# Kernel tuning notes

Measured on AMD Instinct MI355X. Metric: run time of the kernel, lower is better.

Reference implementation:

```python
import jax, jax.numpy as jnp
import numpy as np

N_NODES = 50000
N_EDGES = 800000
NFEAT, NHID, IN_HEAD, NCLASS, OUT_HEAD = 256, 16, 8, 47, 1
NEG_SLOPE = 0.2


def setup_inputs() -> dict:
    key = jax.random.key(0)
    ks = jax.random.split(key, 10)
    x = jax.random.normal(ks[0], (N_NODES, NFEAT), dtype=jnp.float32)
    edge_index = jax.random.randint(ks[1], (2, N_EDGES), 0, N_NODES, dtype=jnp.int64)
    W1 = jax.random.normal(ks[2], (NFEAT, IN_HEAD * NHID), dtype=jnp.float32) * 0.06
    a1_src = jax.random.normal(ks[3], (IN_HEAD, NHID), dtype=jnp.float32) * 0.25
    a1_dst = jax.random.normal(ks[4], (IN_HEAD, NHID), dtype=jnp.float32) * 0.25
    b1 = jax.random.normal(ks[5], (IN_HEAD * NHID,), dtype=jnp.float32) * 0.02
    W2 = jax.random.normal(ks[6], (IN_HEAD * NHID, NCLASS), dtype=jnp.float32) * 0.09
    a2_src = jax.random.normal(ks[7], (OUT_HEAD, NCLASS), dtype=jnp.float32) * 0.15
    a2_dst = jax.random.normal(ks[8], (OUT_HEAD, NCLASS), dtype=jnp.float32) * 0.15
    b2 = jax.random.normal(ks[9], (NCLASS,), dtype=jnp.float32) * 0.02
    return {"x": x, "edge_index": edge_index, "W1": W1, "a1_src": a1_src,
            "a1_dst": a1_dst, "b1": b1, "W2": W2, "a2_src": a2_src,
            "a2_dst": a2_dst, "b2": b2}


def _gat_layer(x, W, a_src, a_dst, b, src, dst, n_nodes, concat):
    # x: [N, F_in]; W: [F_in, H*C]; a_*: [H, C]
    H, C = a_src.shape
    h = (x @ W).reshape(n_nodes, H, C)                        # [N, H, C]
    # per-node partial attention logits, then gather per edge
    s_src = jnp.einsum('nhc,hc->nh', h, a_src)                # [N, H]
    s_dst = jnp.einsum('nhc,hc->nh', h, a_dst)                # [N, H]
    e = jax.nn.leaky_relu(s_src[src] + s_dst[dst], NEG_SLOPE) # [E, H]
    # segment softmax over destination node
    m = jax.ops.segment_max(e, dst, num_segments=n_nodes)     # [N, H]
    ex = jnp.exp(e - m[dst])
    denom = jax.ops.segment_sum(ex, dst, num_segments=n_nodes)
    alpha = ex / (denom[dst] + 1e-16)                         # [E, H]
    # weighted message aggregation (scatter-add)
    msg = alpha[:, :, None] * h[src]                          # [E, H, C]
    out = jax.ops.segment_sum(msg, dst, num_segments=n_nodes) # [N, H, C]
    out = out.reshape(n_nodes, H * C) if concat else out.mean(axis=1)
    return out + b


def reference(x, edge_index, W1, a1_src, a1_dst, b1, W2, a2_src, a2_dst, b2):
    n = x.shape[0]
    # PyG GATConv default: add self-loops
    loops = jnp.arange(n, dtype=edge_index.dtype)
    src = jnp.concatenate([edge_index[0], loops])
    dst = jnp.concatenate([edge_index[1], loops])
    # eval mode: dropout is identity
    h = _gat_layer(x, W1, a1_src, a1_dst, b1, src, dst, n, concat=True)
    h = jax.nn.elu(h)
    out = _gat_layer(h, W2, a2_src, a2_dst, b2, src, dst, n, concat=False)
    return jax.nn.log_softmax(out, axis=1)
```

## Files before the change

kernel.cpp:

```cpp
#include <hip/hip_runtime.h>
#include <hip/hip_fp16.h>

#define N_NODES 50000
#define N_EDGES 800000
#define E2 (N_EDGES + N_NODES)

#define BSHIFT 6
#define BMASK 63
#define NBUCK 782
#define EPB 4096
#define NBLKC 208

typedef _Float16 h8v __attribute__((ext_vector_type(8)));
typedef float f4v __attribute__((ext_vector_type(4)));


__global__ __launch_bounds__(256) void k_hist(const int* __restrict__ ei,
                                              int* __restrict__ gh) {
    __shared__ int h[NBUCK];
    int tid = threadIdx.x;
    for (int b = tid; b < NBUCK; b += 256) h[b] = 0;
    __syncthreads();
    int base = blockIdx.x * EPB;
    for (int i = tid; i < EPB; i += 256) {
        int e = base + i;
        if (e < E2) {
            int dst = (e < N_EDGES) ? ei[N_EDGES + e] : (e - N_EDGES);
            atomicAdd(&h[dst >> BSHIFT], 1);
        }
    }
    __syncthreads();
    for (int b = tid; b < NBUCK; b += 256) gh[blockIdx.x * NBUCK + b] = h[b];
}

__global__ __launch_bounds__(256) void k_colscan(int* __restrict__ gh,
                                                 int* __restrict__ tot) {
    int wave = threadIdx.x >> 6, lane = threadIdx.x & 63;
    int b = blockIdx.x * 4 + wave;
    if (b >= NBUCK) return;
    int carry = 0;
    for (int c = 0; c < NBLKC; c += 64) {
        int k = c + lane;
        int v = (k < NBLKC) ? gh[k * NBUCK + b] : 0;
        int x = v;
        #pragma unroll
        for (int o = 1; o < 64; o <<= 1) { int y = __shfl_up(x, o); if (lane >= o) x += y; }
        if (k < NBLKC) gh[k * NBUCK + b] = carry + x - v;
        carry += __shfl(x, 63);
    }
    if (lane == 0) tot[b] = carry;
}

__global__ __launch_bounds__(1024) void k_btot(const int* __restrict__ tot,
        int* __restrict__ boff, const float* __restrict__ W2, float* __restrict__ W2p) {
    int t = threadIdx.x;
    for (int i = t; i < 128 * 48; i += 1024) {
        int k = i / 48, c = i - k * 48;
        W2p[i] = (c < 47) ? W2[k * 47 + c] : 0.f;
    }
    int v = (t < NBUCK) ? tot[t] : 0;
    __shared__ int ws[16];
    int lane = t & 63, w = t >> 6;
    int x = v;
    #pragma unroll
    for (int o = 1; o < 64; o <<= 1) { int y = __shfl_up(x, o); if (lane >= o) x += y; }
    if (lane == 63) ws[w] = x;
    __syncthreads();
    if (t == 0) {
        #pragma unroll
        for (int j = 1; j < 16; ++j) ws[j] += ws[j - 1];
    }
    __syncthreads();
    int add = (w == 0) ? 0 : ws[w - 1];
    int excl = add + x - v;
    if (t < NBUCK) boff[t] = excl;
    if (t == NBUCK - 1) boff[NBUCK] = excl + v;
}

__global__ __launch_bounds__(256) void k_place(const int* __restrict__ ei,
        const int* __restrict__ gh, const int* __restrict__ boff,
        unsigned int* __restrict__ brec) {
    __shared__ int sbase[NBUCK];
    __shared__ int cnt[NBUCK];
    int tid = threadIdx.x;
    for (int b = tid; b < NBUCK; b += 256) {
        sbase[b] = boff[b] + gh[blockIdx.x * NBUCK + b];
        cnt[b] = 0;
    }
    __syncthreads();
    int base = blockIdx.x * EPB;
    for (int i = tid; i < EPB; i += 256) {
        int e = base + i;
        if (e < E2) {
            int src, dst;
            if (e < N_EDGES) { src = ei[e]; dst = ei[N_EDGES + e]; }
            else             { src = dst = e - N_EDGES; }
            int b = dst >> BSHIFT;
            int r = atomicAdd(&cnt[b], 1);
            brec[sbase[b] + r] = ((unsigned int)(dst & BMASK) << 16) | (unsigned int)src;
        }
    }
}

__global__ __launch_bounds__(256) void k_finalize(const unsigned int* __restrict__ brec,
        const int* __restrict__ boff, unsigned short* __restrict__ csr_src,
        int* __restrict__ offs) {
    int B = blockIdx.x;
    int tid = threadIdx.x;
    int base = boff[B];
    int total = boff[B + 1] - base;
    __shared__ int hist[64], cur[64];
    __shared__ unsigned short stage[2048];
    if (tid < 64) hist[tid] = 0;
    __syncthreads();
    const unsigned int* bp = brec + base;
    for (int i = tid; i < total; i += 256) atomicAdd(&hist[bp[i] >> 16], 1);
    __syncthreads();
    if (tid < 64) {
        int v = hist[tid];
        int x = v;
        #pragma unroll
        for (int o = 1; o < 64; o <<= 1) { int y = __shfl_up(x, o); if (tid >= o) x += y; }
        int excl = x - v;
        cur[tid] = excl;
        int n = B * 64 + tid;
        if (n < N_NODES) offs[n] = base + excl;
    }
    if (B == NBUCK - 1 && tid == 0) offs[N_NODES] = boff[NBUCK];
    __syncthreads();
    if (total <= 2048) {
        for (int i = tid; i < total; i += 256) {
            unsigned int r = bp[i];
            int p = atomicAdd(&cur[r >> 16], 1);
            stage[p] = (unsigned short)(r & 0xFFFFu);
        }
        __syncthreads();
        for (int i = tid; i < total; i += 256) csr_src[base + i] = stage[i];
    } else {
        for (int i = tid; i < total; i += 256) {
            unsigned int r = bp[i];
            int p = atomicAdd(&cur[r >> 16], 1);
            csr_src[base + p] = (unsigned short)(r & 0xFFFFu);
        }
    }
}


__global__ void k_prepw1(const float* __restrict__ W1, _Float16* __restrict__ W1T) {
    int i = blockIdx.x * 256 + threadIdx.x;
    if (i >= 128 * 256) return;
    int c = i >> 8, k = i & 255;
    W1T[i] = (_Float16)W1[k * 128 + c];
}


__global__ __launch_bounds__(128) void k_gemm1(const float* __restrict__ x,
        const _Float16* __restrict__ W1T, _Float16* __restrict__ h1h) {
    int lane = threadIdx.x & 63;
    int wv = threadIdx.x >> 6;
    int rowbase = blockIdx.x * 64 + wv * 32;
    int r0 = lane & 15;
    int kg = lane >> 4;
    f4v acc[2][8];
    #pragma unroll
    for (int i = 0; i < 2; ++i)
        #pragma unroll
        for (int j = 0; j < 8; ++j) acc[i][j] = (f4v)0.f;

    #pragma unroll 1
    for (int kt = 0; kt < 256; kt += 32) {
        h8v a[2];
        #pragma unroll
        for (int rf = 0; rf < 2; ++rf) {
            int row = rowbase + rf * 16 + r0;
            if (row >= N_NODES) row = N_NODES - 1;
            const float* ap = x + (size_t)row * 256 + kt + kg * 8;
            float4 lo = *(const float4*)ap;
            float4 hi = *(const float4*)(ap + 4);
            h8v t;
            t[0] = (_Float16)lo.x; t[1] = (_Float16)lo.y;
            t[2] = (_Float16)lo.z; t[3] = (_Float16)lo.w;
            t[4] = (_Float16)hi.x; t[5] = (_Float16)hi.y;
            t[6] = (_Float16)hi.z; t[7] = (_Float16)hi.w;
            a[rf] = t;
        }
        #pragma unroll
        for (int cf = 0; cf < 8; ++cf) {
            h8v b = *(const h8v*)(W1T + (size_t)(cf * 16 + r0) * 256 + kt + kg * 8);
            acc[0][cf] = __builtin_amdgcn_mfma_f32_16x16x32_f16(a[0], b, acc[0][cf], 0, 0, 0);
            acc[1][cf] = __builtin_amdgcn_mfma_f32_16x16x32_f16(a[1], b, acc[1][cf], 0, 0, 0);
        }
    }
    #pragma unroll
    for (int rf = 0; rf < 2; ++rf) {
        #pragma unroll
        for (int r = 0; r < 4; ++r) {
            int row = rowbase + rf * 16 + kg * 4 + r;
            if (row < N_NODES) {
                _Float16* orow = h1h + (size_t)row * 128 + r0;
                #pragma unroll
                for (int cf = 0; cf < 8; ++cf)
                    orow[cf * 16] = (_Float16)acc[rf][cf][r];
            }
        }
    }
}


__global__ void k_logits1(const __half* __restrict__ h1h,
                          const float* __restrict__ a1s, const float* __restrict__ a1d,
                          float* __restrict__ s1s, float* __restrict__ s1d) {
    int idx = blockIdx.x * blockDim.x + threadIdx.x;
    if (idx >= N_NODES * 8) return;
    int n = idx >> 3, h = idx & 7;
    const __half2* hp2 = (const __half2*)(h1h + (size_t)n * 128 + h * 16);
    float ss = 0.f, sd = 0.f;
    #pragma unroll
    for (int c2 = 0; c2 < 8; ++c2) {
        float2 v = __half22float2(hp2[c2]);
        ss += v.x * a1s[h * 16 + 2 * c2] + v.y * a1s[h * 16 + 2 * c2 + 1];
        sd += v.x * a1d[h * 16 + 2 * c2] + v.y * a1d[h * 16 + 2 * c2 + 1];
    }
    s1s[idx] = ss;
    s1d[idx] = sd;
}


__global__ __launch_bounds__(256) void k_agg1(const __half* __restrict__ h1h,
        const float* __restrict__ s1s, const float* __restrict__ s1d,
        const int* __restrict__ offs, const unsigned short* __restrict__ csr_src,
        const float* __restrict__ b1, float* __restrict__ h2o) {
    int wave = threadIdx.x >> 6;
    int lane = threadIdx.x & 63;
    int n = blockIdx.x * 4 + wave;
    int beg = offs[n];
    int deg = offs[n + 1] - beg;

    int h = lane & 7;
    int slot = lane >> 3;
    int hd = lane >> 3;
    float sdh = s1d[n * 8 + h];

    float dsum = 0.f;
    float accx = 0.f, accy = 0.f;
    for (int chunk = 0; chunk < deg; chunk += 8) {
        int i = chunk + slot;
        int esrc = csr_src[beg + ((i < deg) ? i : (deg - 1))];
        float aN = 0.f;
        if (i < deg) {
            float e = s1s[esrc * 8 + h] + sdh;
            e = (e > 0.f) ? e : 0.2f * e;
            aN = __expf(e);
            dsum += aN;
        }
        int   srcs[8];
        float as[8];
        #pragma unroll
        for (int s = 0; s < 8; ++s) {
            srcs[s] = __shfl(esrc, s * 8);
            as[s]   = __shfl(aN, s * 8 + hd);
        }
        __half2 v[8];
        #pragma unroll
        for (int s = 0; s < 8; ++s)
            v[s] = *(const __half2*)(h1h + (size_t)srcs[s] * 128 + 2 * lane);
        #pragma unroll
        for (int s = 0; s < 8; ++s) {
            float2 vf = __half22float2(v[s]);
            accx += as[s] * vf.x;
            accy += as[s] * vf.y;
        }
    }
    dsum += __shfl_xor(dsum, 8);
    dsum += __shfl_xor(dsum, 16);
    dsum += __shfl_xor(dsum, 32);
    float rd = 1.f / __shfl(dsum, hd);

    float v0 = accx * rd + b1[2 * lane];
    v0 = (v0 > 0.f) ? v0 : (__expf(v0) - 1.f);
    float v1 = accy * rd + b1[2 * lane + 1];
    v1 = (v1 > 0.f) ? v1 : (__expf(v1) - 1.f);
    *(float2*)(h2o + (size_t)n * 128 + 2 * lane) = make_float2(v0, v1);
}


__global__ __launch_bounds__(256) void k_gemm2(const float* __restrict__ h2,
        const float* __restrict__ W2p,
        const float* __restrict__ a2s, const float* __restrict__ a2d,
        __half* __restrict__ g2h, float* __restrict__ s2s, float* __restrict__ s2d) {
    int n = blockIdx.x * 256 + threadIdx.x;
    bool valid = (n < N_NODES);
    int nn = valid ? n : (N_NODES - 1);
    const float* hrow = h2 + (size_t)nn * 128;
    float4 acc[12];
    #pragma unroll
    for (int j = 0; j < 12; ++j) acc[j] = make_float4(0.f, 0.f, 0.f, 0.f);
    #pragma unroll 1
    for (int k = 0; k < 128; k += 4) {
        float4 hv = *(const float4*)(hrow + k);
        float hk[4] = {hv.x, hv.y, hv.z, hv.w};
        #pragma unroll
        for (int kk = 0; kk < 4; ++kk) {
            const float* wrow = W2p + (size_t)(k + kk) * 48;
            #pragma unroll
            for (int j = 0; j < 12; ++j) {
                float4 wv = *(const float4*)(wrow + j * 4);
                acc[j].x += hk[kk] * wv.x;
                acc[j].y += hk[kk] * wv.y;
                acc[j].z += hk[kk] * wv.z;
                acc[j].w += hk[kk] * wv.w;
            }
        }
    }
    float vs = 0.f, vd = 0.f;
    #pragma unroll
    for (int j = 0; j < 12; ++j) {
        int c = j * 4;
        vs += acc[j].x * a2s[c + 0]; vd += acc[j].x * a2d[c + 0];
        vs += acc[j].y * a2s[c + 1]; vd += acc[j].y * a2d[c + 1];
        vs += acc[j].z * a2s[c + 2]; vd += acc[j].z * a2d[c + 2];
        if (j < 11) { vs += acc[j].w * a2s[c + 3]; vd += acc[j].w * a2d[c + 3]; }
    }
    if (valid) {
        __half2* orow = (__half2*)(g2h + (size_t)n * 48);
        #pragma unroll
        for (int j = 0; j < 12; ++j) {
            orow[j * 2 + 0] = __floats2half2_rn(acc[j].x, acc[j].y);
            orow[j * 2 + 1] = __floats2half2_rn(acc[j].z, acc[j].w);
        }
        s2s[n] = vs;
        s2d[n] = vd;
    }
}


__global__ __launch_bounds__(256) void k_agg2(const __half* __restrict__ g2h,
        const float* __restrict__ s2s, const float* __restrict__ s2d,
        const int* __restrict__ offs, const unsigned short* __restrict__ csr_src,
        const float* __restrict__ b2, float* __restrict__ outp) {
    int wave = threadIdx.x >> 6, lane = threadIdx.x & 63;
    int n = blockIdx.x * 4 + wave;
    int beg = offs[n];
    int deg = offs[n + 1] - beg;
    float sdn = s2d[n];
    int c = (lane < 47) ? lane : 47;

    float dsum = 0.f;
    float acc = 0.f;
    for (int chunk = 0; chunk < deg; chunk += 64) {
        int i = chunk + lane;
        int esrc = csr_src[beg + ((i < deg) ? i : (deg - 1))];
        float aN = 0.f;
        if (i < deg) {
            float e = s2s[esrc] + sdn;
            e = (e > 0.f) ? e : 0.2f * e;
            aN = __expf(e);
            dsum += aN;
        }
        int lim = deg - chunk; if (lim > 64) lim = 64;
        for (int g = 0; g < lim; g += 8) {
            int   srcs[8];
            float as[8];
            #pragma unroll
            for (int s = 0; s < 8; ++s) {
                srcs[s] = __shfl(esrc, g + s);
                as[s]   = __shfl(aN, g + s);
            }
            __half v[8];
            #pragma unroll
            for (int s = 0; s < 8; ++s) v[s] = g2h[(size_t)srcs[s] * 48 + c];
            #pragma unroll
            for (int s = 0; s < 8; ++s) acc += as[s] * __half2float(v[s]);
        }
    }
    #pragma unroll
    for (int o = 32; o; o >>= 1) dsum += __shfl_xor(dsum, o);
    acc *= 1.f / dsum;

    float l = (lane < 47) ? acc + b2[lane] : -1e30f;
    float rm = l;
    #pragma unroll
    for (int o = 32; o; o >>= 1) rm = fmaxf(rm, __shfl_xor(rm, o));
    float p = (lane < 47) ? __expf(l - rm) : 0.f;
    float ps = p;
    #pragma unroll
    for (int o = 32; o; o >>= 1) ps += __shfl_xor(ps, o);
    float lse = rm + __logf(ps);
    if (lane < 47) outp[(size_t)n * 47 + lane] = l - lse;
}


extern "C" void kernel_launch(void* const* d_in, const int* in_sizes, int n_in,
                              void* d_out, int out_size, void* d_ws, size_t ws_size,
                              hipStream_t stream) {
    const float* x   = (const float*)d_in[0];
    const int*   ei  = (const int*)d_in[1];
    const float* W1  = (const float*)d_in[2];
    const float* a1s = (const float*)d_in[3];
    const float* a1d = (const float*)d_in[4];
    const float* b1  = (const float*)d_in[5];
    const float* W2  = (const float*)d_in[6];
    const float* a2s = (const float*)d_in[7];
    const float* a2d = (const float*)d_in[8];
    const float* b2  = (const float*)d_in[9];
    float* outp = (float*)d_out;

    char* ws = (char*)d_ws;
    size_t off = 0;
    auto alloc = [&](size_t bytes) -> void* {
        void* p = ws + off;
        off += (bytes + 255) & ~(size_t)255;
        return p;
    };
    int* gh      = (int*)alloc((size_t)NBLKC * NBUCK * 4);
    int* tot     = (int*)alloc((size_t)NBUCK * 4);
    int* boff    = (int*)alloc((size_t)(NBUCK + 1) * 4);
    unsigned int* brec = (unsigned int*)alloc((size_t)E2 * 4);
    unsigned short* csr_src = (unsigned short*)alloc((size_t)E2 * 2);
    int* offs    = (int*)alloc((size_t)(N_NODES + 1) * 4);
    __half* h1h  = (__half*)alloc((size_t)N_NODES * 128 * 2);
    float* s1s   = (float*)alloc((size_t)N_NODES * 8 * 4);
    float* s1d   = (float*)alloc((size_t)N_NODES * 8 * 4);
    float* h2    = (float*)alloc((size_t)N_NODES * 128 * 4);
    __half* g2h  = (__half*)alloc((size_t)N_NODES * 48 * 2);
    float* s2s   = (float*)alloc((size_t)N_NODES * 4);
    float* s2d   = (float*)alloc((size_t)N_NODES * 4);
    float* W2p   = (float*)alloc((size_t)128 * 48 * 4);
    _Float16* W1T = (_Float16*)alloc((size_t)128 * 256 * 2);

    (void)in_sizes; (void)n_in; (void)out_size; (void)ws_size;

    k_prepw1<<<128, 256, 0, stream>>>(W1, W1T);
    k_hist<<<NBLKC, 256, 0, stream>>>(ei, gh);
    k_colscan<<<(NBUCK + 3) / 4, 256, 0, stream>>>(gh, tot);
    k_btot<<<1, 1024, 0, stream>>>(tot, boff, W2, W2p);
    k_place<<<NBLKC, 256, 0, stream>>>(ei, gh, boff, brec);
    k_finalize<<<NBUCK, 256, 0, stream>>>(brec, boff, csr_src, offs);

    k_gemm1<<<(N_NODES + 63) / 64, 128, 0, stream>>>(x, W1T, (_Float16*)h1h);
    k_logits1<<<(N_NODES * 8 + 255) / 256, 256, 0, stream>>>(h1h, a1s, a1d, s1s, s1d);
    k_agg1<<<N_NODES / 4, 256, 0, stream>>>(h1h, s1s, s1d, offs, csr_src, b1, h2);

    k_gemm2<<<(N_NODES + 255) / 256, 256, 0, stream>>>(h2, W2p, a2s, a2d, g2h, s2s, s2d);
    k_agg2<<<N_NODES / 4, 256, 0, stream>>>(g2h, s2s, s2d, offs, csr_src, b2, outp);
}
```

Measured before the change: 181.5 us.

## Split layer-1 aggregation per head, store fp16 head-major h2, fuse W1 prep

The layer-1 aggregation now launches one wave per (node, head): lanes gather 16 channels across four edge groups at once, and the partial sums are reduced with shuffles. The layer-1 output is stored as fp16 in a head-major layout, and gemm2 is changed to read that layout. W1 transpose prep moves into an extra block of the histogram kernel, which removes one launch. This raises parallelism for low-degree nodes and halves h2 traffic. In exchange, the edge list and logits are re-read once per head, the h1h gathers become 32-byte scattered reads, and h2 loses some precision.

```diff
diff --git a/kernel.cpp b/kernel.cpp
--- a/kernel.cpp
+++ b/kernel.cpp
@@ -16,7 +16,14 @@
 
 
 __global__ __launch_bounds__(256) void k_hist(const int* __restrict__ ei,
-                                              int* __restrict__ gh) {
+        int* __restrict__ gh, const float* __restrict__ W1, _Float16* __restrict__ W1T) {
+    if (blockIdx.x == NBLKC) {
+        for (int i = threadIdx.x; i < 128 * 256; i += 256) {
+            int c = i >> 8, k = i & 255;
+            W1T[i] = (_Float16)W1[k * 128 + c];
+        }
+        return;
+    }
     __shared__ int h[NBUCK];
     int tid = threadIdx.x;
     for (int b = tid; b < NBUCK; b += 256) h[b] = 0;
@@ -143,14 +150,6 @@
             csr_src[base + p] = (unsigned short)(r & 0xFFFFu);
         }
     }
-}
-
-
-__global__ void k_prepw1(const float* __restrict__ W1, _Float16* __restrict__ W1T) {
-    int i = blockIdx.x * 256 + threadIdx.x;
-    if (i >= 128 * 256) return;
-    int c = i >> 8, k = i & 255;
-    W1T[i] = (_Float16)W1[k * 128 + c];
 }
 
 
@@ -229,86 +228,81 @@
 __global__ __launch_bounds__(256) void k_agg1(const __half* __restrict__ h1h,
         const float* __restrict__ s1s, const float* __restrict__ s1d,
         const int* __restrict__ offs, const unsigned short* __restrict__ csr_src,
-        const float* __restrict__ b1, float* __restrict__ h2o) {
+        const float* __restrict__ b1, __half* __restrict__ h2s) {
     int wave = threadIdx.x >> 6;
     int lane = threadIdx.x & 63;
-    int n = blockIdx.x * 4 + wave;
+    int s = blockIdx.x & 7;
+    int n = (blockIdx.x >> 3) * 4 + wave;
     int beg = offs[n];
     int deg = offs[n + 1] - beg;
-
-    int h = lane & 7;
-    int slot = lane >> 3;
-    int hd = lane >> 3;
-    float sdh = s1d[n * 8 + h];
+    int c = lane & 15;
+    int grp = lane >> 4;
+    float sdh = s1d[n * 8 + s];
 
     float dsum = 0.f;
-    float accx = 0.f, accy = 0.f;
-    for (int chunk = 0; chunk < deg; chunk += 8) {
-        int i = chunk + slot;
+    float acc = 0.f;
+    for (int chunk = 0; chunk < deg; chunk += 64) {
+        int i = chunk + lane;
         int esrc = csr_src[beg + ((i < deg) ? i : (deg - 1))];
         float aN = 0.f;
         if (i < deg) {
-            float e = s1s[esrc * 8 + h] + sdh;
+            float e = s1s[esrc * 8 + s] + sdh;
             e = (e > 0.f) ? e : 0.2f * e;
             aN = __expf(e);
             dsum += aN;
         }
-        int   srcs[8];
-        float as[8];
-        #pragma unroll
-        for (int s = 0; s < 8; ++s) {
-            srcs[s] = __shfl(esrc, s * 8);
-            as[s]   = __shfl(aN, s * 8 + hd);
-        }
-        __half2 v[8];
-        #pragma unroll
-        for (int s = 0; s < 8; ++s)
-            v[s] = *(const __half2*)(h1h + (size_t)srcs[s] * 128 + 2 * lane);
-        #pragma unroll
-        for (int s = 0; s < 8; ++s) {
-            float2 vf = __half22float2(v[s]);
-            accx += as[s] * vf.x;
-            accy += as[s] * vf.y;
-        }
-    }
-    dsum += __shfl_xor(dsum, 8);
-    dsum += __shfl_xor(dsum, 16);
-    dsum += __shfl_xor(dsum, 32);
-    float rd = 1.f / __shfl(dsum, hd);
-
-    float v0 = accx * rd + b1[2 * lane];
-    v0 = (v0 > 0.f) ? v0 : (__expf(v0) - 1.f);
-    float v1 = accy * rd + b1[2 * lane + 1];
-    v1 = (v1 > 0.f) ? v1 : (__expf(v1) - 1.f);
-    *(float2*)(h2o + (size_t)n * 128 + 2 * lane) = make_float2(v0, v1);
-}
-
-
-__global__ __launch_bounds__(256) void k_gemm2(const float* __restrict__ h2,
+        int rem = deg - chunk; if (rem > 64) rem = 64;
+        int lim = (rem + 3) >> 2;
+        for (int st = 0; st < lim; ++st) {
+            int j = st * 4 + grp;
+            int src = __shfl(esrc, j);
+            float w = __shfl(aN, j);
+            float v = __half2float(h1h[(size_t)src * 128 + s * 16 + c]);
+            acc += w * v;
+        }
+    }
+    #pragma unroll
+    for (int o = 32; o; o >>= 1) dsum += __shfl_xor(dsum, o);
+    acc += __shfl_xor(acc, 16);
+    acc += __shfl_xor(acc, 32);
+    float rd = 1.f / dsum;
+    if (lane < 16) {
+        float v = acc * rd + b1[s * 16 + c];
+        v = (v > 0.f) ? v : (__expf(v) - 1.f);
+        h2s[((size_t)s * N_NODES + n) * 16 + c] = __float2half_rn(v);
+    }
+}
+
+
+__global__ __launch_bounds__(256) void k_gemm2(const __half* __restrict__ h2s,
         const float* __restrict__ W2p,
         const float* __restrict__ a2s, const float* __restrict__ a2d,
         __half* __restrict__ g2h, float* __restrict__ s2s, float* __restrict__ s2d) {
     int n = blockIdx.x * 256 + threadIdx.x;
     bool valid = (n < N_NODES);
     int nn = valid ? n : (N_NODES - 1);
-    const float* hrow = h2 + (size_t)nn * 128;
     float4 acc[12];
     #pragma unroll
     for (int j = 0; j < 12; ++j) acc[j] = make_float4(0.f, 0.f, 0.f, 0.f);
     #pragma unroll 1
-    for (int k = 0; k < 128; k += 4) {
-        float4 hv = *(const float4*)(hrow + k);
-        float hk[4] = {hv.x, hv.y, hv.z, hv.w};
-        #pragma unroll
-        for (int kk = 0; kk < 4; ++kk) {
-            const float* wrow = W2p + (size_t)(k + kk) * 48;
+    for (int s8 = 0; s8 < 8; ++s8) {
+        const __half2* hp = (const __half2*)(h2s + ((size_t)s8 * N_NODES + nn) * 16);
+        #pragma unroll
+        for (int q = 0; q < 8; ++q) {
+            float2 hv = __half22float2(hp[q]);
+            float hk[2] = {hv.x, hv.y};
             #pragma unroll
-            for (int j = 0; j < 12; ++j) {
-                float4 wv = *(const float4*)(wrow + j * 4);
-                acc[j].x += hk[kk] * wv.x;
-                acc[j].y += hk[kk] * wv.y;
-                acc[j].z += hk[kk] * wv.z;
-                acc[j].w += hk[kk] * wv.w;
+            for (int t2 = 0; t2 < 2; ++t2) {
+                int k = s8 * 16 + q * 2 + t2;
+                const float* wrow = W2p + (size_t)k * 48;
+                #pragma unroll
+                for (int j = 0; j < 12; ++j) {
+                    float4 wv = *(const float4*)(wrow + j * 4);
+                    acc[j].x += hk[t2] * wv.x;
+                    acc[j].y += hk[t2] * wv.y;
+                    acc[j].z += hk[t2] * wv.z;
+                    acc[j].w += hk[t2] * wv.w;
+                }
             }
         }
     }
@@ -421,7 +415,7 @@
     __half* h1h  = (__half*)alloc((size_t)N_NODES * 128 * 2);
     float* s1s   = (float*)alloc((size_t)N_NODES * 8 * 4);
     float* s1d   = (float*)alloc((size_t)N_NODES * 8 * 4);
-    float* h2    = (float*)alloc((size_t)N_NODES * 128 * 4);
+    __half* h2s  = (__half*)alloc((size_t)N_NODES * 128 * 2);
     __half* g2h  = (__half*)alloc((size_t)N_NODES * 48 * 2);
     float* s2s   = (float*)alloc((size_t)N_NODES * 4);
     float* s2d   = (float*)alloc((size_t)N_NODES * 4);
@@ -430,8 +424,7 @@
 
     (void)in_sizes; (void)n_in; (void)out_size; (void)ws_size;
 
-    k_prepw1<<<128, 256, 0, stream>>>(W1, W1T);
-    k_hist<<<NBLKC, 256, 0, stream>>>(ei, gh);
+    k_hist<<<NBLKC + 1, 256, 0, stream>>>(ei, gh, W1, W1T);
     k_colscan<<<(NBUCK + 3) / 4, 256, 0, stream>>>(gh, tot);
     k_btot<<<1, 1024, 0, stream>>>(tot, boff, W2, W2p);
     k_place<<<NBLKC, 256, 0, stream>>>(ei, gh, boff, brec);
@@ -439,8 +432,8 @@
 
     k_gemm1<<<(N_NODES + 63) / 64, 128, 0, stream>>>(x, W1T, (_Float16*)h1h);
     k_logits1<<<(N_NODES * 8 + 255) / 256, 256, 0, stream>>>(h1h, a1s, a1d, s1s, s1d);
-    k_agg1<<<N_NODES / 4, 256, 0, stream>>>(h1h, s1s, s1d, offs, csr_src, b1, h2);
-
-    k_gemm2<<<(N_NODES + 255) / 256, 256, 0, stream>>>(h2, W2p, a2s, a2d, g2h, s2s, s2d);
+    k_agg1<<<(N_NODES / 4) * 8, 256, 0, stream>>>(h1h, s1s, s1d, offs, csr_src, b1, h2s);
+
+    k_gemm2<<<(N_NODES + 255) / 256, 256, 0, stream>>>(h2s, W2p, a2s, a2d, g2h, s2s, s2d);
     k_agg2<<<N_NODES / 4, 256, 0, stream>>>(g2h, s2s, s2d, offs, csr_src, b2, outp);
 }
```

Result: slower. 353.1 us, median of 2 (+94.6%).
